# Kernel optimization log

Measured on AMD Instinct MI355X. Metric: run time of the kernel, lower is better.

The kernel has to match this reference:

```python
import jax, jax.numpy as jnp
import numpy as np

N_QUBITS = 12
DEPTH = 2
TOPOLOGY = 'ring'
N_FEATURES = 12
BATCH = 4096
DIM = 2 ** N_QUBITS


def _apply_ry(state, theta):
    # state: [B, left, 2, right] caller-reshaped; here take [B, 2**n] + qubit index
    return state


def apply_ry(state, theta, q):
    # RY(theta) = [[cos(t/2), -sin(t/2)], [sin(t/2), cos(t/2)]], shared across batch
    c, s = jnp.cos(theta / 2), jnp.sin(theta / 2)
    G = jnp.stack([jnp.stack([c, -s]), jnp.stack([s, c])])  # [2, 2]
    left = 2 ** q
    right = 2 ** (N_QUBITS - q - 1)
    st = state.reshape(-1, left, 2, right)
    st = jnp.einsum('ab,xlbr->xlar', G, st)
    return st.reshape(state.shape)


def apply_cnot(state, c, t):
    # flip target axis on the control=1 half of the statevector
    B = state.shape[0]
    st = state.reshape((B,) + (2,) * N_QUBITS)
    c_ax, t_ax = 1 + c, 1 + t
    s0 = jnp.take(st, 0, axis=c_ax)
    s1 = jnp.take(st, 1, axis=c_ax)
    t_adj = t_ax if t < c else t_ax - 1  # axis shift after removing control axis
    s1 = jnp.flip(s1, axis=t_adj)
    st = jnp.stack([s0, s1], axis=c_ax)
    return st.reshape(B, DIM)


def circuit_features(x, weights):
    B = x.shape[0]
    # initial layer: RY(x[i % n_features]) on |0> per qubit -> product state
    idx = np.arange(N_QUBITS) % N_FEATURES
    half = x[:, idx] / 2  # [B, n_qubits]
    state = jnp.ones((B, 1), dtype=x.dtype)
    for i in range(N_QUBITS):
        v = jnp.stack([jnp.cos(half[:, i]), jnp.sin(half[:, i])], axis=1)  # [B, 2]
        state = (state[:, :, None] * v[:, None, :]).reshape(B, -1)
    # entangling + trainable RY layers
    for l in range(DEPTH):
        if TOPOLOGY == 'ring':
            pairs = [(i, (i + 1) % N_QUBITS) for i in range(N_QUBITS)]
        elif TOPOLOGY == 'chain':
            pairs = [(i, i + 1) for i in range(N_QUBITS - 1)]
        else:  # all2all
            pairs = [(i, j) for i in range(N_QUBITS) for j in range(i + 1, N_QUBITS)]
        for (ci, ti) in pairs:
            state = apply_cnot(state, ci, ti)
        for i in range(N_QUBITS):
            state = apply_ry(state, weights[l, i], i)
    # <Z_i> = sum_b |amp_b|^2 * (1 - 2*bit_i(b)); qubit 0 is most significant
    probs = state * state  # [B, 2^n], state is real
    bits = (np.arange(DIM)[None, :] >> (N_QUBITS - 1 - np.arange(N_QUBITS))[:, None]) & 1
    signs = jnp.asarray(1.0 - 2.0 * bits, dtype=x.dtype)  # [n_qubits, 2^n]
    return probs @ signs.T  # [B, n_qubits]


def setup_inputs() -> dict:
    key = jax.random.key(0)
    kx, kw, kW, kb = jax.random.split(key, 4)
    x = jax.random.normal(kx, (BATCH, N_FEATURES), dtype=jnp.float32)
    weights = jax.random.normal(kw, (DEPTH, N_QUBITS), dtype=jnp.float32)
    W = jax.random.normal(kW, (2, N_QUBITS), dtype=jnp.float32) / np.sqrt(N_QUBITS)
    b = jnp.zeros((2,), dtype=jnp.float32)
    return {"x": x, "weights": weights, "W": W, "b": b}


def reference(x, weights, W, b):
    feats = circuit_features(x, weights)  # [B, n_qubits]
    return feats @ W.T + b  # [B, 2]
```

## Files before the change

### kernel.cpp

```cpp
#include <hip/hip_runtime.h>
#include <hip/hip_bf16.h>

#define NQ 12
typedef __hip_bfloat16 bf16;
typedef float v2f __attribute__((ext_vector_type(2)));

__device__ __forceinline__ float b2f(unsigned int u) {
  union { unsigned int i; float f; } v; v.i = u << 16; return v.f;
}

__device__ __forceinline__ float ldv(const void* p, int i, bool f32) {
  if (f32) return ((const float*)p)[i];
  return b2f((unsigned int)((const unsigned short*)p)[i]);
}

__device__ __forceinline__ int ringperm(int d) {
  int a = d ^ ((d & 1) << 11);
  return a ^ (a >> 1);
}

__device__ __forceinline__ int swz(int p) { return p ^ ((p >> 6) & 31); }

__global__ __launch_bounds__(64) void qsim_kernel(
    const void* __restrict__ x,
    const void* __restrict__ w,
    const void* __restrict__ Wm,
    const void* __restrict__ bv,
    void* __restrict__ out)
{
  __shared__ float st[4096];
  const int lane = threadIdx.x;
  const int b = blockIdx.x;

  bool f32;
  {
    const unsigned short* xu = (const unsigned short*)x;
    int insane = 0;
#pragma unroll
    for (int i = 0; i < 16; ++i) {
      float v = b2f((unsigned int)xu[2 * i]);
      float a = fabsf(v);
      if (!(a <= 64.f) || (a != 0.f && a < 1e-8f)) ++insane;
    }
    f32 = (insane >= 2);
  }

  v2f amp[32];
  {
    float csx[12], snx[12];
#pragma unroll
    for (int q = 0; q < 12; ++q) {
      float h = 0.5f * ldv(x, b * NQ + q, f32);
      csx[q] = __cosf(h); snx[q] = __sinf(h);
    }
    const int rb = ringperm(lane << 6);
    float f0[12], f1[12];
#pragma unroll
    for (int q = 0; q < 12; ++q) {
      int r = (rb >> (11 - q)) & 1;
      f0[q] = r ? snx[q] : csx[q];
      f1[q] = r ? csx[q] : snx[q];
    }
    const float K   = f0[2] * f0[3] * f0[4] * f0[5];
    const float h0f = f0[0] * f0[1];
    const float h1f = f1[0] * f1[1];
    const float u00 = f0[11] * h0f, u01 = f1[11] * h1f;
    const float u10 = f1[11] * h0f, u11 = f0[11] * h1f;
#pragma unroll
    for (int j5 = 0; j5 < 2; ++j5) {
      const float a5 = K * (j5 ? f1[6] : f0[6]);
#pragma unroll
      for (int j4 = 0; j4 < 2; ++j4) {
        const float a4 = a5 * ((j4 ^ j5) ? f1[7] : f0[7]);
#pragma unroll
        for (int j3 = 0; j3 < 2; ++j3) {
          const float a3 = a4 * ((j3 ^ j4) ? f1[8] : f0[8]);
#pragma unroll
          for (int j2 = 0; j2 < 2; ++j2) {
            const float a2 = a3 * ((j2 ^ j3) ? f1[9] : f0[9]);
#pragma unroll
            for (int j1 = 0; j1 < 2; ++j1) {
              const float a1 = a2 * ((j1 ^ j2) ? f1[10] : f0[10]);
              const int k = (j5 << 4) | (j4 << 3) | (j3 << 2) | (j2 << 1) | j1;
              amp[k].x = a1 * (j1 ? u10 : u00);
              amp[k].y = a1 * (j1 ? u11 : u01);
            }
          }
        }
      }
    }
  }

  const int rb1 = swz(ringperm(lane << 6));
  const int wb2 = (lane << 6) ^ (lane & 31);

#pragma unroll
  for (int q = 6; q < 11; ++q) {
    float h = 0.5f * ldv(w, 0 * NQ + q, f32);
    const float t = __tanf(0.5f * h), s = __sinf(h);
    const int hm = 1 << (10 - q);
#pragma unroll
    for (int k = 0; k < 32; ++k) {
      if (k & hm) continue;
      amp[k]      += -t * amp[k | hm];
      amp[k | hm] +=  s * amp[k];
      amp[k]      += -t * amp[k | hm];
    }
  }
  {
    float h = 0.5f * ldv(w, 0 * NQ + 11, f32);
    const float t = __tanf(0.5f * h), s = __sinf(h);
#pragma unroll
    for (int k = 0; k < 32; ++k) {
      amp[k].x = fmaf(-t, amp[k].y, amp[k].x);
      amp[k].y = fmaf( s, amp[k].x, amp[k].y);
      amp[k].x = fmaf(-t, amp[k].y, amp[k].x);
    }
  }

  __syncthreads();
#pragma unroll
  for (int j = 0; j < 64; ++j)
    st[wb2 ^ j] = amp[j >> 1][j & 1];
  __syncthreads();
#pragma unroll
  for (int j = 0; j < 64; ++j)
    amp[j >> 1][j & 1] = st[((j << 6) ^ (j & 31)) ^ lane];

#pragma unroll
  for (int q = 0; q < 5; ++q) {
    float h = 0.5f * ldv(w, 0 * NQ + q, f32);
    const float t = __tanf(0.5f * h), s = __sinf(h);
    const int hm = 1 << (4 - q);
#pragma unroll
    for (int k = 0; k < 32; ++k) {
      if (k & hm) continue;
      amp[k]      += -t * amp[k | hm];
      amp[k | hm] +=  s * amp[k];
      amp[k]      += -t * amp[k | hm];
    }
  }
  {
    float h = 0.5f * ldv(w, 0 * NQ + 5, f32);
    const float t = __tanf(0.5f * h), s = __sinf(h);
#pragma unroll
    for (int k = 0; k < 32; ++k) {
      amp[k].x = fmaf(-t, amp[k].y, amp[k].x);
      amp[k].y = fmaf( s, amp[k].x, amp[k].y);
      amp[k].x = fmaf(-t, amp[k].y, amp[k].x);
    }
  }

  __syncthreads();
#pragma unroll
  for (int j = 0; j < 64; ++j)
    st[((j << 6) ^ (j & 31)) ^ lane] = amp[j >> 1][j & 1];
  __syncthreads();
#pragma unroll
  for (int j = 0; j < 64; ++j)
    amp[j >> 1][j & 1] = st[rb1 ^ swz(ringperm(j))];

  float xB6, xB7, xB8, xB9, xB10, xB11;
  {
    v2f a6 = {0.f, 0.f}, a7 = a6, a8 = a6, a9 = a6, a10 = a6;
    float a11 = 0.f;
#pragma unroll
    for (int k = 0; k < 32; ++k) {
      if (!(k & 16)) a6  += amp[k] * amp[k | 16];
      if (!(k & 8))  a7  += amp[k] * amp[k | 8];
      if (!(k & 4))  a8  += amp[k] * amp[k | 4];
      if (!(k & 2))  a9  += amp[k] * amp[k | 2];
      if (!(k & 1))  a10 += amp[k] * amp[k | 1];
      a11 += amp[k].x * amp[k].y;
    }
    xB6 = 2.f * (a6.x + a6.y);  xB7 = 2.f * (a7.x + a7.y);
    xB8 = 2.f * (a8.x + a8.y);  xB9 = 2.f * (a9.x + a9.y);
    xB10 = 2.f * (a10.x + a10.y); xB11 = 2.f * a11;
  }

  __syncthreads();
#pragma unroll
  for (int j = 0; j < 64; ++j)
    st[wb2 ^ j] = amp[j >> 1][j & 1];
  __syncthreads();
#pragma unroll
  for (int j = 0; j < 64; ++j)
    amp[j >> 1][j & 1] = st[((j << 6) ^ (j & 31)) ^ lane];

  float xA0, xA1, xA2, xA3, xA4, xA5;
  {
    v2f a0 = {0.f, 0.f}, a1 = a0, a2 = a0, a3 = a0, a4 = a0;
    float a5 = 0.f;
#pragma unroll
    for (int k = 0; k < 32; ++k) {
      if (!(k & 16)) a0 += amp[k] * amp[k | 16];
      if (!(k & 8))  a1 += amp[k] * amp[k | 8];
      if (!(k & 4))  a2 += amp[k] * amp[k | 4];
      if (!(k & 2))  a3 += amp[k] * amp[k | 2];
      if (!(k & 1))  a4 += amp[k] * amp[k | 1];
      a5 += amp[k].x * amp[k].y;
    }
    xA0 = 2.f * (a0.x + a0.y);  xA1 = 2.f * (a1.x + a1.y);
    xA2 = 2.f * (a2.x + a2.y);  xA3 = 2.f * (a3.x + a3.y);
    xA4 = 2.f * (a4.x + a4.y);  xA5 = 2.f * a5;
  }

  v2f Pv = {0.f, 0.f}, zv0 = Pv, zv1 = Pv, zv2 = Pv, zv3 = Pv, zv4 = Pv;
  float z5 = 0.f;
#pragma unroll
  for (int k = 0; k < 32; ++k) {
    v2f pr = amp[k] * amp[k];
    Pv += pr;
    zv0 += (k & 16) ? -pr : pr;
    zv1 += (k & 8)  ? -pr : pr;
    zv2 += (k & 4)  ? -pr : pr;
    zv3 += (k & 2)  ? -pr : pr;
    zv4 += (k & 1)  ? -pr : pr;
    z5  += pr.x - pr.y;
  }
  const float P  = Pv.x + Pv.y;
  const float z0 = zv0.x + zv0.y, z1 = zv1.x + zv1.y, z2 = zv2.x + zv2.y;
  const float z3 = zv3.x + zv3.y, z4 = zv4.x + zv4.y;

  float ct[12], sn[12];
#pragma unroll
  for (int q = 0; q < 12; ++q) {
    float th = ldv(w, NQ + q, f32);
    ct[q] = __cosf(th); sn[q] = __sinf(th);
  }
  const float zA[6] = {z0, z1, z2, z3, z4, z5};
  const float xA[6] = {xA0, xA1, xA2, xA3, xA4, xA5};
  const float xB[6] = {xB6, xB7, xB8, xB9, xB10, xB11};

  float t0, t1;
#pragma unroll
  for (int r = 0; r < 2; ++r) {
    float acc = 0.f, wsum = 0.f;
#pragma unroll
    for (int q = 0; q < 6; ++q) {
      float wv = ldv(Wm, r * NQ + q, f32);
      acc = fmaf(wv, fmaf(ct[q], zA[q], -sn[q] * xA[q]), acc);
    }
#pragma unroll
    for (int q = 6; q < 12; ++q) {
      float wv = ldv(Wm, r * NQ + q, f32);
      float wc = wv * ct[q];
      wsum += ((lane >> (11 - q)) & 1) ? -wc : wc;
      acc = fmaf(-wv * sn[q], xB[q - 6], acc);
    }
    acc = fmaf(P, wsum, acc);
    if (r == 0) t0 = acc; else t1 = acc;
  }
#pragma unroll
  for (int off = 32; off; off >>= 1) {
    t0 += __shfl_xor(t0, off, 64);
    t1 += __shfl_xor(t1, off, 64);
  }
  if (lane < 2) {
    float o = ((lane == 0) ? t0 : t1) + ldv(bv, lane, f32);
    if (f32) ((float*)out)[b * 2 + lane] = o;
    else     ((bf16*)out)[b * 2 + lane] = __float2bfloat16(o);
  }
}

extern "C" void kernel_launch(void* const* d_in, const int* in_sizes, int n_in,
                              void* d_out, int out_size, void* d_ws, size_t ws_size,
                              hipStream_t stream) {
  const void* x  = d_in[0];
  const void* w  = d_in[1];
  const void* Wm = d_in[2];
  const void* bv = d_in[3];
  const int batch = out_size / 2;
  qsim_kernel<<<dim3(batch), dim3(64), 0, stream>>>(x, w, Wm, bv, d_out);
}
```

Baseline: 84.13 us.

## Halve LDS buffer with two-phase transposes and raise occupancy bound

Shrinks the shared-memory statevector buffer from 4096 to 2048 floats. Each register-to-LDS transpose now runs in two halves, with the lanes split so that each phase fits in the smaller buffer, and adds a launch-bounds hint of 4 waves. The aim is to fit more blocks per CU by cutting LDS use and registers. In exchange it doubles the barriers and LDS passes per transpose, and the trig and W loads are fused into a single epilogue loop.

New measurement: 163.4 us. +94.2%, slower.

```diff
diff --git a/kernel.cpp b/kernel.cpp
--- a/kernel.cpp
+++ b/kernel.cpp
@@ -21,14 +21,14 @@
 
 __device__ __forceinline__ int swz(int p) { return p ^ ((p >> 6) & 31); }
 
-__global__ __launch_bounds__(64) void qsim_kernel(
+__global__ __launch_bounds__(64, 4) void qsim_kernel(
     const void* __restrict__ x,
     const void* __restrict__ w,
     const void* __restrict__ Wm,
     const void* __restrict__ bv,
     void* __restrict__ out)
 {
-  __shared__ float st[4096];
+  __shared__ float st[2048];
   const int lane = threadIdx.x;
   const int b = blockIdx.x;
 
@@ -47,19 +47,15 @@
 
   v2f amp[32];
   {
-    float csx[12], snx[12];
+    const int rb = ringperm(lane << 6);
+    float f0[12], f1[12];
 #pragma unroll
     for (int q = 0; q < 12; ++q) {
       float h = 0.5f * ldv(x, b * NQ + q, f32);
-      csx[q] = __cosf(h); snx[q] = __sinf(h);
-    }
-    const int rb = ringperm(lane << 6);
-    float f0[12], f1[12];
-#pragma unroll
-    for (int q = 0; q < 12; ++q) {
+      float c = __cosf(h), s = __sinf(h);
       int r = (rb >> (11 - q)) & 1;
-      f0[q] = r ? snx[q] : csx[q];
-      f1[q] = r ? csx[q] : snx[q];
+      f0[q] = r ? s : c;
+      f1[q] = r ? c : s;
     }
     const float K   = f0[2] * f0[3] * f0[4] * f0[5];
     const float h0f = f0[0] * f0[1];
@@ -92,7 +88,6 @@
   }
 
   const int rb1 = swz(ringperm(lane << 6));
-  const int wb2 = (lane << 6) ^ (lane & 31);
 
 #pragma unroll
   for (int q = 6; q < 11; ++q) {
@@ -119,13 +114,45 @@
   }
 
   __syncthreads();
-#pragma unroll
-  for (int j = 0; j < 64; ++j)
-    st[wb2 ^ j] = amp[j >> 1][j & 1];
-  __syncthreads();
-#pragma unroll
-  for (int j = 0; j < 64; ++j)
-    amp[j >> 1][j & 1] = st[((j << 6) ^ (j & 31)) ^ lane];
+  if (lane < 32) {
+#pragma unroll
+    for (int j = 0; j < 32; ++j)
+      st[((lane << 6) ^ (lane & 31) ^ j) & 2047] = amp[j >> 1][j & 1];
+  } else {
+#pragma unroll
+    for (int j = 32; j < 64; ++j)
+      st[((lane << 6) ^ (lane & 31) ^ j) & 2047] = amp[j >> 1][j & 1];
+  }
+  __syncthreads();
+  if (lane < 32) {
+#pragma unroll
+    for (int j = 0; j < 32; ++j)
+      amp[j >> 1][j & 1] = st[(((j << 6) ^ (j & 31)) ^ lane) & 2047];
+  } else {
+#pragma unroll
+    for (int j = 32; j < 64; ++j)
+      amp[j >> 1][j & 1] = st[(((j << 6) ^ (j & 31)) ^ lane) & 2047];
+  }
+  __syncthreads();
+  if (lane < 32) {
+#pragma unroll
+    for (int j = 32; j < 64; ++j)
+      st[((lane << 6) ^ (lane & 31) ^ j) & 2047] = amp[j >> 1][j & 1];
+  } else {
+#pragma unroll
+    for (int j = 0; j < 32; ++j)
+      st[((lane << 6) ^ (lane & 31) ^ j) & 2047] = amp[j >> 1][j & 1];
+  }
+  __syncthreads();
+  if (lane < 32) {
+#pragma unroll
+    for (int j = 32; j < 64; ++j)
+      amp[j >> 1][j & 1] = st[(((j << 6) ^ (j & 31)) ^ lane) & 2047];
+  } else {
+#pragma unroll
+    for (int j = 0; j < 32; ++j)
+      amp[j >> 1][j & 1] = st[(((j << 6) ^ (j & 31)) ^ lane) & 2047];
+  }
 
 #pragma unroll
   for (int q = 0; q < 5; ++q) {
@@ -152,13 +179,53 @@
   }
 
   __syncthreads();
-#pragma unroll
-  for (int j = 0; j < 64; ++j)
-    st[((j << 6) ^ (j & 31)) ^ lane] = amp[j >> 1][j & 1];
-  __syncthreads();
-#pragma unroll
-  for (int j = 0; j < 64; ++j)
-    amp[j >> 1][j & 1] = st[rb1 ^ swz(ringperm(j))];
+  if ((lane & 16) == 0) {
+#pragma unroll
+    for (int j = 0; j < 64; ++j) {
+      if (((j >> 4) ^ (j >> 5)) & 1) continue;
+      st[((((j << 6) ^ (j & 31)) ^ lane)) & 2047] = amp[j >> 1][j & 1];
+    }
+  } else {
+#pragma unroll
+    for (int j = 16; j < 48; ++j)
+      st[((((j << 6) ^ (j & 31)) ^ lane)) & 2047] = amp[j >> 1][j & 1];
+  }
+  __syncthreads();
+  if ((lane & 16) == 0) {
+#pragma unroll
+    for (int j = 0; j < 64; ++j) {
+      if (((j >> 4) ^ (j >> 5)) & 1) continue;
+      amp[j >> 1][j & 1] = st[(rb1 ^ swz(ringperm(j))) & 2047];
+    }
+  } else {
+#pragma unroll
+    for (int j = 16; j < 48; ++j)
+      amp[j >> 1][j & 1] = st[(rb1 ^ swz(ringperm(j))) & 2047];
+  }
+  __syncthreads();
+  if ((lane & 16) == 0) {
+#pragma unroll
+    for (int j = 16; j < 48; ++j)
+      st[((((j << 6) ^ (j & 31)) ^ lane)) & 2047] = amp[j >> 1][j & 1];
+  } else {
+#pragma unroll
+    for (int j = 0; j < 64; ++j) {
+      if (((j >> 4) ^ (j >> 5)) & 1) continue;
+      st[((((j << 6) ^ (j & 31)) ^ lane)) & 2047] = amp[j >> 1][j & 1];
+    }
+  }
+  __syncthreads();
+  if ((lane & 16) == 0) {
+#pragma unroll
+    for (int j = 16; j < 48; ++j)
+      amp[j >> 1][j & 1] = st[(rb1 ^ swz(ringperm(j))) & 2047];
+  } else {
+#pragma unroll
+    for (int j = 0; j < 64; ++j) {
+      if (((j >> 4) ^ (j >> 5)) & 1) continue;
+      amp[j >> 1][j & 1] = st[(rb1 ^ swz(ringperm(j))) & 2047];
+    }
+  }
 
   float xB6, xB7, xB8, xB9, xB10, xB11;
   {
@@ -179,13 +246,45 @@
   }
 
   __syncthreads();
-#pragma unroll
-  for (int j = 0; j < 64; ++j)
-    st[wb2 ^ j] = amp[j >> 1][j & 1];
-  __syncthreads();
-#pragma unroll
-  for (int j = 0; j < 64; ++j)
-    amp[j >> 1][j & 1] = st[((j << 6) ^ (j & 31)) ^ lane];
+  if (lane < 32) {
+#pragma unroll
+    for (int j = 0; j < 32; ++j)
+      st[((lane << 6) ^ (lane & 31) ^ j) & 2047] = amp[j >> 1][j & 1];
+  } else {
+#pragma unroll
+    for (int j = 32; j < 64; ++j)
+      st[((lane << 6) ^ (lane & 31) ^ j) & 2047] = amp[j >> 1][j & 1];
+  }
+  __syncthreads();
+  if (lane < 32) {
+#pragma unroll
+    for (int j = 0; j < 32; ++j)
+      amp[j >> 1][j & 1] = st[(((j << 6) ^ (j & 31)) ^ lane) & 2047];
+  } else {
+#pragma unroll
+    for (int j = 32; j < 64; ++j)
+      amp[j >> 1][j & 1] = st[(((j << 6) ^ (j & 31)) ^ lane) & 2047];
+  }
+  __syncthreads();
+  if (lane < 32) {
+#pragma unroll
+    for (int j = 32; j < 64; ++j)
+      st[((lane << 6) ^ (lane & 31) ^ j) & 2047] = amp[j >> 1][j & 1];
+  } else {
+#pragma unroll
+    for (int j = 0; j < 32; ++j)
+      st[((lane << 6) ^ (lane & 31) ^ j) & 2047] = amp[j >> 1][j & 1];
+  }
+  __syncthreads();
+  if (lane < 32) {
+#pragma unroll
+    for (int j = 32; j < 64; ++j)
+      amp[j >> 1][j & 1] = st[(((j << 6) ^ (j & 31)) ^ lane) & 2047];
+  } else {
+#pragma unroll
+    for (int j = 0; j < 32; ++j)
+      amp[j >> 1][j & 1] = st[(((j << 6) ^ (j & 31)) ^ lane) & 2047];
+  }
 
   float xA0, xA1, xA2, xA3, xA4, xA5;
   {
@@ -222,35 +321,34 @@
   const float z0 = zv0.x + zv0.y, z1 = zv1.x + zv1.y, z2 = zv2.x + zv2.y;
   const float z3 = zv3.x + zv3.y, z4 = zv4.x + zv4.y;
 
-  float ct[12], sn[12];
-#pragma unroll
-  for (int q = 0; q < 12; ++q) {
-    float th = ldv(w, NQ + q, f32);
-    ct[q] = __cosf(th); sn[q] = __sinf(th);
-  }
   const float zA[6] = {z0, z1, z2, z3, z4, z5};
   const float xA[6] = {xA0, xA1, xA2, xA3, xA4, xA5};
   const float xB[6] = {xB6, xB7, xB8, xB9, xB10, xB11};
 
-  float t0, t1;
-#pragma unroll
-  for (int r = 0; r < 2; ++r) {
-    float acc = 0.f, wsum = 0.f;
-#pragma unroll
-    for (int q = 0; q < 6; ++q) {
-      float wv = ldv(Wm, r * NQ + q, f32);
-      acc = fmaf(wv, fmaf(ct[q], zA[q], -sn[q] * xA[q]), acc);
-    }
-#pragma unroll
-    for (int q = 6; q < 12; ++q) {
-      float wv = ldv(Wm, r * NQ + q, f32);
-      float wc = wv * ct[q];
-      wsum += ((lane >> (11 - q)) & 1) ? -wc : wc;
-      acc = fmaf(-wv * sn[q], xB[q - 6], acc);
-    }
-    acc = fmaf(P, wsum, acc);
-    if (r == 0) t0 = acc; else t1 = acc;
-  }
+  float t0 = 0.f, t1 = 0.f, ws0 = 0.f, ws1 = 0.f;
+#pragma unroll
+  for (int q = 0; q < 12; ++q) {
+    const float th = ldv(w, NQ + q, f32);
+    const float c = __cosf(th), s = __sinf(th);
+    const float w0 = ldv(Wm, q, f32);
+    const float w1 = ldv(Wm, NQ + q, f32);
+    if (q < 6) {
+      const float zx = fmaf(c, zA[q], -s * xA[q]);
+      t0 = fmaf(w0, zx, t0);
+      t1 = fmaf(w1, zx, t1);
+    } else {
+      const float sx = -s * xB[q - 6];
+      t0 = fmaf(w0, sx, t0);
+      t1 = fmaf(w1, sx, t1);
+      const float c0 = w0 * c, c1 = w1 * c;
+      const bool neg = (lane >> (11 - q)) & 1;
+      ws0 += neg ? -c0 : c0;
+      ws1 += neg ? -c1 : c1;
+    }
+  }
+  t0 = fmaf(P, ws0, t0);
+  t1 = fmaf(P, ws1, t1);
+
 #pragma unroll
   for (int off = 32; off; off >>= 1) {
     t0 += __shfl_xor(t0, off, 64);
```
